# Performance work log

Hardware: AMD Instinct MI355X
Metric: run time of the kernel (lower is better)

## Reference

```python
import jax, jax.numpy as jnp
import numpy as np

DIM = 128
HALF = DIM // 2
K = 8
B_TAIL = 1.0
MIN_W = 1e-3
MIN_H = 1e-3
MIN_D = 1e-3


def _fcnn(x, w1, b1, w2, b2, w3, b3):
    h = jax.nn.silu(x @ w1 + b1)
    h = jax.nn.silu(h @ w2 + b2)
    return h @ w3 + b3


def _rqs_forward(x, uw, uh, ud):
    # x: (B, D); uw/uh: (B, D, K); ud: (B, D, K-1)
    inside = (x >= -B_TAIL) & (x <= B_TAIL)
    const = np.log(np.exp(1.0 - MIN_D) - 1.0).astype(np.float32)
    ud = jnp.pad(ud, ((0, 0), (0, 0), (1, 1)), constant_values=const)

    widths = jax.nn.softmax(uw, axis=-1)
    widths = MIN_W + (1.0 - MIN_W * K) * widths
    cumw = jnp.pad(jnp.cumsum(widths, axis=-1), ((0, 0), (0, 0), (1, 0)))
    cumw = 2.0 * B_TAIL * cumw - B_TAIL
    cumw = cumw.at[..., 0].set(-B_TAIL).at[..., -1].set(B_TAIL)
    widths = cumw[..., 1:] - cumw[..., :-1]

    derivs = MIN_D + jax.nn.softplus(ud)

    heights = jax.nn.softmax(uh, axis=-1)
    heights = MIN_H + (1.0 - MIN_H * K) * heights
    cumh = jnp.pad(jnp.cumsum(heights, axis=-1), ((0, 0), (0, 0), (1, 0)))
    cumh = 2.0 * B_TAIL * cumh - B_TAIL
    cumh = cumh.at[..., 0].set(-B_TAIL).at[..., -1].set(B_TAIL)
    heights = cumh[..., 1:] - cumh[..., :-1]

    # searchsorted on cumwidths (forward direction)
    locs = cumw.at[..., -1].add(1e-6)
    idx = jnp.sum(x[..., None] >= locs, axis=-1) - 1
    idx = jnp.clip(idx, 0, K - 1)[..., None]  # (B, D, 1)

    g = lambda a: jnp.take_along_axis(a, idx, axis=-1)[..., 0]
    in_cumw = g(cumw)
    in_w = g(widths)
    in_cumh = g(cumh)
    in_h = g(heights)
    in_delta = g(heights / widths)
    d0 = g(derivs)
    d1 = g(derivs[..., 1:])

    theta = (x - in_cumw) / in_w
    t1mt = theta * (1.0 - theta)
    numer = in_h * (in_delta * theta * theta + d0 * t1mt)
    denom = in_delta + (d0 + d1 - 2.0 * in_delta) * t1mt
    out = in_cumh + numer / denom
    dnum = in_delta * in_delta * (d1 * theta * theta + 2.0 * in_delta * t1mt + d0 * (1.0 - theta) ** 2)
    lad = jnp.log(dnum) - 2.0 * jnp.log(denom)

    out = jnp.where(inside, out, x)
    lad = jnp.where(inside, lad, 0.0)
    return out, lad


def _forward(x, f1, f2):
    lower, upper = x[:, :HALF], x[:, HALF:]
    out = _fcnn(lower, *f1).reshape(-1, DIM - HALF, 3 * K - 1)
    W, H, D = out[..., :K], out[..., K:2 * K], out[..., 2 * K:]
    upper, ld1 = _rqs_forward(upper, W, H, D)
    out = _fcnn(upper, *f2).reshape(-1, HALF, 3 * K - 1)
    W, H, D = out[..., :K], out[..., K:2 * K], out[..., 2 * K:]
    lower, ld2 = _rqs_forward(lower, W, H, D)
    log_det = jnp.sum(ld1, axis=1) + jnp.sum(ld2, axis=1)
    return jnp.concatenate([lower, upper], axis=1), log_det


def setup_inputs() -> dict:
    key = jax.random.key(0)
    ks = jax.random.split(key, 13)
    batch = 32768
    x = jax.random.uniform(ks[0], (batch, DIM), jnp.float32, -1.2, 1.2)
    hd = 512
    out_dim = (3 * K - 1) * HALF  # 1472

    def lin(k, fan_in, fan_out):
        bound = 1.0 / np.sqrt(fan_in)
        kw, kb = jax.random.split(k)
        w = jax.random.uniform(kw, (fan_in, fan_out), jnp.float32, -bound, bound)
        b = jax.random.uniform(kb, (fan_out,), jnp.float32, -bound, bound)
        return w, b

    f1_w1, f1_b1 = lin(ks[1], HALF, hd)
    f1_w2, f1_b2 = lin(ks[2], hd, hd)
    f1_w3, f1_b3 = lin(ks[3], hd, out_dim)
    f2_w1, f2_b1 = lin(ks[4], HALF, hd)
    f2_w2, f2_b2 = lin(ks[5], hd, hd)
    f2_w3, f2_b3 = lin(ks[6], hd, out_dim)
    return dict(x=x,
                f1_w1=f1_w1, f1_b1=f1_b1, f1_w2=f1_w2, f1_b2=f1_b2, f1_w3=f1_w3, f1_b3=f1_b3,
                f2_w1=f2_w1, f2_b1=f2_b1, f2_w2=f2_w2, f2_b2=f2_b2, f2_w3=f2_w3, f2_b3=f2_b3)


def reference(x, f1_w1, f1_b1, f1_w2, f1_b2, f1_w3, f1_b3,
              f2_w1, f2_b1, f2_w2, f2_b2, f2_w3, f2_b3):
    f1 = (f1_w1, f1_b1, f1_w2, f1_b2, f1_w3, f1_b3)
    f2 = (f2_w1, f2_b1, f2_w2, f2_b2, f2_w3, f2_b3)
    return _forward(x, f1, f2)
```

## Files before the change

kernel.cpp:

```cpp
#include <hip/hip_runtime.h>

#define DIM 128
#define HALF 64

typedef __attribute__((ext_vector_type(8))) short bf16x8;
typedef __attribute__((ext_vector_type(4))) float f32x4;

static __device__ __forceinline__ float bf2f(unsigned int u16) {
    unsigned int v = u16 << 16;
    return __builtin_bit_cast(float, v);
}
static __device__ __forceinline__ unsigned short f2bf(float f) {
    unsigned int u = __builtin_bit_cast(unsigned int, f);
    unsigned int r = 0x7fffu + ((u >> 16) & 1u);
    u += r;
    return (unsigned short)(u >> 16);
}

static __device__ __forceinline__ void gload_lds16(const void* gptr, void* ldsptr) {
    __builtin_amdgcn_global_load_lds(
        (const __attribute__((address_space(1))) unsigned int*)(uintptr_t)gptr,
        (__attribute__((address_space(3))) unsigned int*)(unsigned int)(uintptr_t)ldsptr,
        16, 0, 0);
}

#define RAW_BARRIER()  __builtin_amdgcn_s_barrier()
#define SCHED_FENCE()  __builtin_amdgcn_sched_barrier(0)
#define WAIT_LGKM0()   asm volatile("s_waitcnt lgkmcnt(0)" ::: "memory")
#define WAIT_VM(n)     asm volatile("s_waitcnt vmcnt(" #n ")" ::: "memory")


__global__ void conv_lower_kernel(const float* __restrict__ x,
                                  unsigned short* __restrict__ xl, int batch) {
    int i = blockIdx.x * 256 + threadIdx.x;
    if (i < batch * HALF) {
        int r = i >> 6, c = i & 63;
        xl[i] = f2bf(x[(size_t)r * DIM + c]);
    }
}

struct TransDesc {
    const float* src[6];
    unsigned short* dst[6];
};

__global__ void transpose_all_kernel(TransDesc d) {
    __shared__ float tile[32][33];
    int z = blockIdx.z;
    int K, BN, BK, Nin, pad24;
    switch (z) {
        case 0: case 3: K = 64;  BK = 2;  BN = 16; Nin = 512;  pad24 = 0; break;
        case 1: case 4: K = 512; BK = 16; BN = 16; Nin = 512;  pad24 = 0; break;
        default:        K = 512; BK = 16; BN = 48; Nin = 1472; pad24 = 1; break;
    }
    int bn = blockIdx.x, bk = blockIdx.y;
    if (bn >= BN || bk >= BK) return;
    const float* w = d.src[z];
    unsigned short* wt = d.dst[z];
    int tx = threadIdx.x, ty = threadIdx.y;
#pragma unroll
    for (int i = 0; i < 4; ++i) {
        int k = bk * 32 + ty + 8 * i;
        int n = bn * 32 + tx;
        float v = 0.f;
        if (pad24) {
            int g = n / 24, cc = n % 24;
            if (cc < 23) v = w[(size_t)k * Nin + (g * 23 + cc)];
        } else {
            v = w[(size_t)k * Nin + n];
        }
        tile[ty + 8 * i][tx] = v;
    }
    __syncthreads();
#pragma unroll
    for (int i = 0; i < 4; ++i) {
        int n = bn * 32 + ty + 8 * i;
        int k = bk * 32 + tx;
        wt[(size_t)n * K + k] = f2bf(tile[tx][ty + 8 * i]);
    }
}

template <bool SILU, int NT>
__global__ __launch_bounds__(256, 4) void gemm_bf16_kernel(
    const unsigned short* __restrict__ A, const unsigned short* __restrict__ Bt,
    const float* __restrict__ bias, unsigned short* __restrict__ C,
    int M, int N, int K) {
    __shared__ __align__(16) unsigned char smem[34816];
    unsigned short* a_lds = (unsigned short*)smem;
    unsigned short* b_lds = (unsigned short*)(smem + 16384);
    unsigned short* cbuf = (unsigned short*)smem;

    const int t = threadIdx.x;
    const int lane = t & 63;
    const int wid = t >> 6;
    const int wr = wid >> 1, wc = wid & 1;

    const int nwg = gridDim.x;
    const int b = blockIdx.x;
    const int id = ((nwg & 7) == 0) ? ((b & 7) * (nwg >> 3) + (b >> 3)) : b;
    const int m0 = (id / NT) * 128;
    const int n0 = (id % NT) * 128;

    const int l15 = lane & 15;
    const int l4 = lane >> 4;
    const int srow = lane >> 3;
    const int sseg = lane & 7;
    const int sseg_swz = sseg ^ srow;
    const int rswz = (l15 & 7) * 8;

    f32x4 acc[4][4] = {};

    for (int kt = 0; kt < K; kt += 64) {
#pragma unroll
        for (int i = 0; i < 4; ++i) {
            int chunk = wid * 4 + i;
            int row = chunk * 8 + srow;
            const unsigned short* gA = A + (size_t)(m0 + row) * K + kt + sseg_swz * 8;
            const unsigned short* gB = Bt + (size_t)(n0 + row) * K + kt + sseg_swz * 8;
            gload_lds16(gA, &a_lds[chunk * 512]);
            gload_lds16(gB, &b_lds[chunk * 512]);
        }
        __syncthreads();
#pragma unroll
        for (int k0 = 0; k0 < 2; ++k0) {
            bf16x8 af[4], bfv[4];
#pragma unroll
            for (int f = 0; f < 4; ++f) {
                int col = (k0 * 32 + l4 * 8) ^ rswz;
                af[f] = *reinterpret_cast<const bf16x8*>(
                    &a_lds[(wr * 64 + f * 16 + l15) * 64 + col]);
                bfv[f] = *reinterpret_cast<const bf16x8*>(
                    &b_lds[(wc * 64 + f * 16 + l15) * 64 + col]);
            }
#pragma unroll
            for (int fm = 0; fm < 4; ++fm)
#pragma unroll
                for (int fn = 0; fn < 4; ++fn)
                    acc[fm][fn] = __builtin_amdgcn_mfma_f32_16x16x32_bf16(
                        af[fm], bfv[fn], acc[fm][fn], 0, 0, 0);
        }
        __syncthreads();
    }

    float bv[4];
#pragma unroll
    for (int fn = 0; fn < 4; ++fn) bv[fn] = bias[n0 + wc * 64 + fn * 16 + l15];
#pragma unroll
    for (int fm = 0; fm < 4; ++fm) {
#pragma unroll
        for (int r = 0; r < 4; ++r) {
            int rl = wr * 64 + fm * 16 + l4 * 4 + r;
#pragma unroll
            for (int fn = 0; fn < 4; ++fn) {
                float v = acc[fm][fn][r] + bv[fn];
                if (SILU) v = v / (1.f + __expf(-v));
                cbuf[rl * 136 + wc * 64 + fn * 16 + l15] = f2bf(v);
            }
        }
    }
    __syncthreads();
#pragma unroll
    for (int p = 0; p < 8; ++p) {
        int unit = p * 256 + t;
        int row = unit >> 4, seg = unit & 15;
        uint4 v = *reinterpret_cast<const uint4*>(&cbuf[row * 136 + seg * 8]);
        *reinterpret_cast<uint4*>(&C[(size_t)(m0 + row) * N + n0 + seg * 8]) = v;
    }
}

template <bool SILU, bool PAD24, int NT>
__global__ __launch_bounds__(512, 1) void gemm256_kernel(
    const unsigned short* __restrict__ A, const unsigned short* __restrict__ Bt,
    const float* __restrict__ bias, unsigned short* __restrict__ C,
    int M, int N, int K) {
    __shared__ __align__(16) unsigned short lds[256 * 264];

    const int t = threadIdx.x;
    const int lane = t & 63;
    const int wid = t >> 6;
    const int wr = wid >> 2;
    const int wc = wid & 3;
    const int l15 = lane & 15;
    const int l4 = lane >> 4;

    const int nwg = gridDim.x;
    const int b = blockIdx.x;
    const int id = ((nwg & 7) == 0) ? ((b & 7) * (nwg >> 3) + (b >> 3)) : b;
    const int m0 = (id / NT) * 256;
    const int n0 = (id % NT) * 256;

    const int nkt = K >> 5;

    const int arow0 = t >> 2;
    const int arow1 = 128 + (t >> 2);
    const int aslot0 = (t & 3) ^ ((arow0 >> 1) & 3);
    const int aslot1 = (t & 3) ^ ((arow1 >> 1) & 3);
    const int wbase0 = wid * 512;
    const int wbase1 = 4096 + wid * 512;

    int aoff[8], boff[4];
#pragma unroll
    for (int f = 0; f < 8; ++f) {
        int row = wr * 128 + f * 16 + l15;
        aoff[f] = row * 32 + ((l4 ^ ((row >> 1) & 3)) * 8);
    }
#pragma unroll
    for (int g = 0; g < 4; ++g) {
        int row = wc * 64 + g * 16 + l15;
        boff[g] = 8192 + row * 32 + ((l4 ^ ((row >> 1) & 3)) * 8);
    }

    f32x4 acc[8][4] = {};

    auto stageA = [&](int u) {
        const int bi = (u % 3) * 16384;
        const unsigned short* Au = A + (size_t)m0 * K + u * 32;
        gload_lds16(Au + (size_t)arow0 * K + aslot0 * 8, &lds[bi + wbase0]);
        gload_lds16(Au + (size_t)arow1 * K + aslot1 * 8, &lds[bi + wbase1]);
    };
    auto stageB = [&](int u) {
        const int bi = (u % 3) * 16384 + 8192;
        const unsigned short* Bu = Bt + (size_t)n0 * K + u * 32;
        gload_lds16(Bu + (size_t)arow0 * K + aslot0 * 8, &lds[bi + wbase0]);
        gload_lds16(Bu + (size_t)arow1 * K + aslot1 * 8, &lds[bi + wbase1]);
    };

    stageA(0); stageB(0); stageA(1); stageB(1);
    WAIT_VM(4);
    RAW_BARRIER();
    SCHED_FENCE();

    for (int kt = 0; kt < nkt; ++kt) {
        const int bi = (kt % 3) * 16384;
        const bool st = (kt + 2 < nkt);

        bf16x8 bfv[4], af[4];
#pragma unroll
        for (int g = 0; g < 4; ++g)
            bfv[g] = *reinterpret_cast<const bf16x8*>(&lds[bi + boff[g]]);
#pragma unroll
        for (int f = 0; f < 4; ++f)
            af[f] = *reinterpret_cast<const bf16x8*>(&lds[bi + aoff[f]]);
        if (st) stageA(kt + 2);
        RAW_BARRIER();
        WAIT_LGKM0();
        SCHED_FENCE();
        __builtin_amdgcn_s_setprio(1);
#pragma unroll
        for (int fm = 0; fm < 4; ++fm)
#pragma unroll
            for (int fn = 0; fn < 4; ++fn)
                acc[fm][fn] = __builtin_amdgcn_mfma_f32_16x16x32_bf16(
                    af[fm], bfv[fn], acc[fm][fn], 0, 0, 0);
        __builtin_amdgcn_s_setprio(0);
        RAW_BARRIER();
        SCHED_FENCE();

        bf16x8 af2[4];
#pragma unroll
        for (int f = 0; f < 4; ++f)
            af2[f] = *reinterpret_cast<const bf16x8*>(&lds[bi + aoff[4 + f]]);
        if (st) stageB(kt + 2);
        RAW_BARRIER();
        WAIT_LGKM0();
        SCHED_FENCE();
        __builtin_amdgcn_s_setprio(1);
#pragma unroll
        for (int fm = 0; fm < 4; ++fm)
#pragma unroll
            for (int fn = 0; fn < 4; ++fn)
                acc[4 + fm][fn] = __builtin_amdgcn_mfma_f32_16x16x32_bf16(
                    af2[fm], bfv[fn], acc[4 + fm][fn], 0, 0, 0);
        __builtin_amdgcn_s_setprio(0);
        if (st) { WAIT_VM(4); } else { WAIT_VM(0); }
        RAW_BARRIER();
        SCHED_FENCE();
    }

    unsigned short* cbuf = lds;
    float bv[4];
#pragma unroll
    for (int fn = 0; fn < 4; ++fn) {
        int n = n0 + wc * 64 + fn * 16 + l15;
        if (PAD24) {
            int g = n / 24, cc = n % 24;
            bv[fn] = (cc < 23) ? bias[g * 23 + cc] : 0.f;
        } else {
            bv[fn] = bias[n];
        }
    }
#pragma unroll
    for (int fm = 0; fm < 8; ++fm) {
#pragma unroll
        for (int r = 0; r < 4; ++r) {
            int rl = wr * 128 + fm * 16 + l4 * 4 + r;
#pragma unroll
            for (int fn = 0; fn < 4; ++fn) {
                float v = acc[fm][fn][r] + bv[fn];
                if (SILU) v = v / (1.f + __expf(-v));
                cbuf[rl * 264 + wc * 64 + fn * 16 + l15] = f2bf(v);
            }
        }
    }
    __syncthreads();
#pragma unroll
    for (int p = 0; p < 16; ++p) {
        int unit = p * 512 + t;
        int row = unit >> 5, seg = unit & 31;
        uint4 v = *reinterpret_cast<const uint4*>(&cbuf[row * 264 + seg * 8]);
        *reinterpret_cast<uint4*>(&C[(size_t)(m0 + row) * N + n0 + seg * 8]) = v;
    }
}

__global__ __launch_bounds__(256, 1) void rqs_kernel(
        const float* __restrict__ x,
        const unsigned short* __restrict__ P,
        float* __restrict__ out, unsigned short* __restrict__ out_bf,
        float* __restrict__ ld_buf, float* __restrict__ logdet_out,
        int xoff, int pass, int batch) {
    const int wid = threadIdx.x >> 6;
    const int lane = threadIdx.x & 63;
    const int r = blockIdx.x * 4 + wid;
    if (r >= batch) return;

    const uint4* pv = reinterpret_cast<const uint4*>(P + (size_t)r * 1536 + lane * 24);
    uint4 q0 = pv[0], q1 = pv[1], q2 = pv[2];

    float W[8], H[8], Dv[7];
    {
        unsigned int a;
        a = q0.x; W[0] = bf2f(a & 0xffff); W[1] = bf2f(a >> 16);
        a = q0.y; W[2] = bf2f(a & 0xffff); W[3] = bf2f(a >> 16);
        a = q0.z; W[4] = bf2f(a & 0xffff); W[5] = bf2f(a >> 16);
        a = q0.w; W[6] = bf2f(a & 0xffff); W[7] = bf2f(a >> 16);
        a = q1.x; H[0] = bf2f(a & 0xffff); H[1] = bf2f(a >> 16);
        a = q1.y; H[2] = bf2f(a & 0xffff); H[3] = bf2f(a >> 16);
        a = q1.z; H[4] = bf2f(a & 0xffff); H[5] = bf2f(a >> 16);
        a = q1.w; H[6] = bf2f(a & 0xffff); H[7] = bf2f(a >> 16);
        a = q2.x; Dv[0] = bf2f(a & 0xffff); Dv[1] = bf2f(a >> 16);
        a = q2.y; Dv[2] = bf2f(a & 0xffff); Dv[3] = bf2f(a >> 16);
        a = q2.z; Dv[4] = bf2f(a & 0xffff); Dv[5] = bf2f(a >> 16);
        a = q2.w; Dv[6] = bf2f(a & 0xffff);
    }

    float cw[9], ch[9];
    {
        float m = W[0];
#pragma unroll
        for (int i = 1; i < 8; ++i) m = fmaxf(m, W[i]);
        float e[8], s = 0.f;
#pragma unroll
        for (int i = 0; i < 8; ++i) { e[i] = __expf(W[i] - m); s += e[i]; }
        float inv = __builtin_amdgcn_rcpf(s), cum = 0.f;
        cw[0] = -1.f;
#pragma unroll
        for (int i = 0; i < 8; ++i) {
            cum += 0.001f + 0.992f * e[i] * inv;
            cw[i + 1] = 2.f * cum - 1.f;
        }
        cw[8] = 1.f;
    }
    {
        float m = H[0];
#pragma unroll
        for (int i = 1; i < 8; ++i) m = fmaxf(m, H[i]);
        float e[8], s = 0.f;
#pragma unroll
        for (int i = 0; i < 8; ++i) { e[i] = __expf(H[i] - m); s += e[i]; }
        float inv = __builtin_amdgcn_rcpf(s), cum = 0.f;
        ch[0] = -1.f;
#pragma unroll
        for (int i = 0; i < 8; ++i) {
            cum += 0.001f + 0.992f * e[i] * inv;
            ch[i + 1] = 2.f * cum - 1.f;
        }
        ch[8] = 1.f;
    }
    float dv[9];
    dv[0] = 1.f; dv[8] = 1.f;
#pragma unroll
    for (int i = 0; i < 7; ++i) {
        float d = Dv[i];
        dv[i + 1] = 0.001f + fmaxf(d, 0.f) + __logf(1.f + __expf(-fabsf(d)));
    }

    const float xv = x[(size_t)r * DIM + xoff + lane];

    int cnt = (xv >= -1.f) ? 1 : 0;
#pragma unroll
    for (int i = 1; i < 8; ++i) cnt += (xv >= cw[i]) ? 1 : 0;
    cnt += (xv >= 1.000001f) ? 1 : 0;
    int idx = cnt - 1;
    idx = idx < 0 ? 0 : (idx > 7 ? 7 : idx);

    float in_cumw = -1.f, in_w = 1.f, in_cumh = -1.f, in_h = 1.f, d0 = 1.f, d1 = 1.f;
#pragma unroll
    for (int i = 0; i < 8; ++i) {
        bool s = (idx == i);
        float wi = cw[i + 1] - cw[i];
        float hi = ch[i + 1] - ch[i];
        in_cumw = s ? cw[i] : in_cumw;
        in_w = s ? wi : in_w;
        in_cumh = s ? ch[i] : in_cumh;
        in_h = s ? hi : in_h;
        d0 = s ? dv[i] : d0;
        d1 = s ? dv[i + 1] : d1;
    }

    float rw = __builtin_amdgcn_rcpf(in_w);
    float in_delta = in_h * rw;
    float theta = (xv - in_cumw) * rw;
    float omt = 1.f - theta;
    float t1mt = theta * omt;
    float numer = in_h * (in_delta * theta * theta + d0 * t1mt);
    float denom = in_delta + (d0 + d1 - 2.f * in_delta) * t1mt;
    float rd = __builtin_amdgcn_rcpf(denom);
    float outv = in_cumh + numer * rd;
    float dnum = in_delta * in_delta *
                 (d1 * theta * theta + 2.f * in_delta * t1mt + d0 * omt * omt);
    float lad = __logf(dnum * rd * rd);

    bool inside = (xv >= -1.f) && (xv <= 1.f);
    outv = inside ? outv : xv;
    lad = inside ? lad : 0.f;

    out[(size_t)r * DIM + xoff + lane] = outv;
    if (pass == 1) out_bf[(size_t)r * HALF + lane] = f2bf(outv);

#pragma unroll
    for (int off = 32; off > 0; off >>= 1) lad += __shfl_xor(lad, off);

    if (lane == 0) {
        if (pass == 1) ld_buf[r] = lad;
        else logdet_out[r] = lad + ld_buf[r];
    }
}


extern "C" void kernel_launch(void* const* d_in, const int* in_sizes, int n_in,
                              void* d_out, int out_size, void* d_ws, size_t ws_size,
                              hipStream_t stream) {
    const float* x = (const float*)d_in[0];
    const float* f1w1 = (const float*)d_in[1];
    const float* f1b1 = (const float*)d_in[2];
    const float* f1w2 = (const float*)d_in[3];
    const float* f1b2 = (const float*)d_in[4];
    const float* f1w3 = (const float*)d_in[5];
    const float* f1b3 = (const float*)d_in[6];
    const float* f2w1 = (const float*)d_in[7];
    const float* f2b1 = (const float*)d_in[8];
    const float* f2w2 = (const float*)d_in[9];
    const float* f2b2 = (const float*)d_in[10];
    const float* f2w3 = (const float*)d_in[11];
    const float* f2b3 = (const float*)d_in[12];
    const int batch = in_sizes[0] / DIM;
    float* out = (float*)d_out;

    char* ws = (char*)d_ws;
    size_t off = 0;
    auto alloc = [&](size_t bytes) -> void* {
        void* p = ws + off;
        off += (bytes + 255) & ~(size_t)255;
        return p;
    };
    unsigned short* xl = (unsigned short*)alloc((size_t)batch * 64 * 2);
    unsigned short* ub = (unsigned short*)alloc((size_t)batch * 64 * 2);
    unsigned short* w1t1 = (unsigned short*)alloc(512 * 64 * 2);
    unsigned short* w2t1 = (unsigned short*)alloc(512 * 512 * 2);
    unsigned short* w3t1 = (unsigned short*)alloc(1536 * 512 * 2);
    unsigned short* w1t2 = (unsigned short*)alloc(512 * 64 * 2);
    unsigned short* w2t2 = (unsigned short*)alloc(512 * 512 * 2);
    unsigned short* w3t2 = (unsigned short*)alloc(1536 * 512 * 2);
    unsigned short* h1 = (unsigned short*)alloc((size_t)batch * 512 * 2);
    unsigned short* h2 = (unsigned short*)alloc((size_t)batch * 512 * 2);
    unsigned short* par = (unsigned short*)alloc((size_t)batch * 1536 * 2);
    float* ld1 = (float*)alloc((size_t)batch * 4);
    (void)ws_size; (void)n_in; (void)out_size;

    conv_lower_kernel<<<(batch * 64 + 255) / 256, 256, 0, stream>>>(x, xl, batch);
    TransDesc td;
    td.src[0] = f1w1; td.dst[0] = w1t1;
    td.src[1] = f1w2; td.dst[1] = w2t1;
    td.src[2] = f1w3; td.dst[2] = w3t1;
    td.src[3] = f2w1; td.dst[3] = w1t2;
    td.src[4] = f2w2; td.dst[4] = w2t2;
    td.src[5] = f2w3; td.dst[5] = w3t2;
    transpose_all_kernel<<<dim3(48, 16, 6), dim3(32, 8), 0, stream>>>(td);

    const int MB128 = batch / 128;
    const int MB256 = batch / 256;
    gemm_bf16_kernel<true, 4><<<MB128 * 4, 256, 0, stream>>>(xl, w1t1, f1b1, h1, batch, 512, 64);
    gemm256_kernel<true, false, 2><<<MB256 * 2, 512, 0, stream>>>(h1, w2t1, f1b2, h2, batch, 512, 512);
    gemm256_kernel<false, true, 6><<<MB256 * 6, 512, 0, stream>>>(h2, w3t1, f1b3, par, batch, 1536, 512);
    rqs_kernel<<<batch / 4, 256, 0, stream>>>(x, par, out, ub, ld1, nullptr, HALF, 1, batch);
    gemm_bf16_kernel<true, 4><<<MB128 * 4, 256, 0, stream>>>(ub, w1t2, f2b1, h1, batch, 512, 64);
    gemm256_kernel<true, false, 2><<<MB256 * 2, 512, 0, stream>>>(h1, w2t2, f2b2, h2, batch, 512, 512);
    gemm256_kernel<false, true, 6><<<MB256 * 6, 512, 0, stream>>>(h2, w3t2, f2b3, par, batch, 1536, 512);
    rqs_kernel<<<batch / 4, 256, 0, stream>>>(x, par, out, nullptr, ld1, out + (size_t)batch * DIM, 0, 2, batch);
}
```

Measured before the change: 378.4 us.

## Simplify GEMM main loop to single phase with one barrier per k-tile

Replaces the two-phase ping-pong main loop, which split A and B staging across halves with extra barriers, explicit lgkm waits and scheduling fences, with a single phase. Each iteration now issues all prefetch loads for tile kt+2 at the top, reads all eight A fragments and four B fragments, runs all 32 MFMAs, then waits and barriers once. This removes barrier and fence overhead and gives the compiler freedom to interleave LDS reads with MFMAs. In exchange it loses the hand-tuned interleaving across waves and raises register pressure from holding eight A fragments at once.

Result: no change. 380.0 us (+0.4%).

```diff
diff --git a/kernel.cpp b/kernel.cpp
--- a/kernel.cpp
+++ b/kernel.cpp
@@ -25,8 +25,6 @@
 }
 
 #define RAW_BARRIER()  __builtin_amdgcn_s_barrier()
-#define SCHED_FENCE()  __builtin_amdgcn_sched_barrier(0)
-#define WAIT_LGKM0()   asm volatile("s_waitcnt lgkmcnt(0)" ::: "memory")
 #define WAIT_VM(n)     asm volatile("s_waitcnt vmcnt(" #n ")" ::: "memory")
 
 
@@ -212,69 +210,43 @@
 
     f32x4 acc[8][4] = {};
 
-    auto stageA = [&](int u) {
+    auto stage = [&](int u) {
         const int bi = (u % 3) * 16384;
         const unsigned short* Au = A + (size_t)m0 * K + u * 32;
+        const unsigned short* Bu = Bt + (size_t)n0 * K + u * 32;
         gload_lds16(Au + (size_t)arow0 * K + aslot0 * 8, &lds[bi + wbase0]);
         gload_lds16(Au + (size_t)arow1 * K + aslot1 * 8, &lds[bi + wbase1]);
+        gload_lds16(Bu + (size_t)arow0 * K + aslot0 * 8, &lds[bi + 8192 + wbase0]);
+        gload_lds16(Bu + (size_t)arow1 * K + aslot1 * 8, &lds[bi + 8192 + wbase1]);
     };
-    auto stageB = [&](int u) {
-        const int bi = (u % 3) * 16384 + 8192;
-        const unsigned short* Bu = Bt + (size_t)n0 * K + u * 32;
-        gload_lds16(Bu + (size_t)arow0 * K + aslot0 * 8, &lds[bi + wbase0]);
-        gload_lds16(Bu + (size_t)arow1 * K + aslot1 * 8, &lds[bi + wbase1]);
-    };
-
-    stageA(0); stageB(0); stageA(1); stageB(1);
+
+    stage(0); stage(1);
     WAIT_VM(4);
     RAW_BARRIER();
-    SCHED_FENCE();
 
     for (int kt = 0; kt < nkt; ++kt) {
+        if (kt + 2 < nkt) stage(kt + 2);
+
         const int bi = (kt % 3) * 16384;
-        const bool st = (kt + 2 < nkt);
-
-        bf16x8 bfv[4], af[4];
+        bf16x8 af[8], bfv[4];
 #pragma unroll
         for (int g = 0; g < 4; ++g)
             bfv[g] = *reinterpret_cast<const bf16x8*>(&lds[bi + boff[g]]);
 #pragma unroll
-        for (int f = 0; f < 4; ++f)
+        for (int f = 0; f < 8; ++f)
             af[f] = *reinterpret_cast<const bf16x8*>(&lds[bi + aoff[f]]);
-        if (st) stageA(kt + 2);
-        RAW_BARRIER();
-        WAIT_LGKM0();
-        SCHED_FENCE();
+
         __builtin_amdgcn_s_setprio(1);
 #pragma unroll
-        for (int fm = 0; fm < 4; ++fm)
+        for (int fm = 0; fm < 8; ++fm)
 #pragma unroll
             for (int fn = 0; fn < 4; ++fn)
                 acc[fm][fn] = __builtin_amdgcn_mfma_f32_16x16x32_bf16(
                     af[fm], bfv[fn], acc[fm][fn], 0, 0, 0);
         __builtin_amdgcn_s_setprio(0);
+
+        if (kt + 2 < nkt) { WAIT_VM(4); } else { WAIT_VM(0); }
         RAW_BARRIER();
-        SCHED_FENCE();
-
-        bf16x8 af2[4];
-#pragma unroll
-        for (int f = 0; f < 4; ++f)
-            af2[f] = *reinterpret_cast<const bf16x8*>(&lds[bi + aoff[4 + f]]);
-        if (st) stageB(kt + 2);
-        RAW_BARRIER();
-        WAIT_LGKM0();
-        SCHED_FENCE();
-        __builtin_amdgcn_s_setprio(1);
-#pragma unroll
-        for (int fm = 0; fm < 4; ++fm)
-#pragma unroll
-            for (int fn = 0; fn < 4; ++fn)
-                acc[4 + fm][fn] = __builtin_amdgcn_mfma_f32_16x16x32_bf16(
-                    af2[fm], bfv[fn], acc[4 + fm][fn], 0, 0, 0);
-        __builtin_amdgcn_s_setprio(0);
-        if (st) { WAIT_VM(4); } else { WAIT_VM(0); }
-        RAW_BARRIER();
-        SCHED_FENCE();
     }
 
     unsigned short* cbuf = lds;
```
